# Kernel tuning notes

Measured on AMD Instinct MI355X. Metric: run time of the kernel, lower is better.

## Reference

```python
import jax, jax.numpy as jnp
import numpy as np

B, D, UNITS = 32768, 1024, 1024
NB_FACTOR, SPARSITY = 3, 32
NB = D // SPARSITY  # 32 blocks of 32x32 per block-diagonal factor


def _block_t_matmul(kb, y):
    # kb: [nb, bi, bo] block-diagonal factor values; y: [nb*bi, batch]
    # computes blockdiag(kb)^T @ y without materializing the dense matrix
    nb, bi, bo = kb.shape
    yb = y.reshape(nb, bi, -1)                      # [nb, bi, batch]
    out = jnp.einsum('nio,nib->nob', kb, yb)        # [nb, bo, batch]
    return out.reshape(nb * bo, -1)


def setup_inputs() -> dict:
    key = jax.random.key(0)
    ks = jax.random.split(key, 9)
    return {
        'x': jax.random.normal(ks[0], (B, D), jnp.float32),
        'P0': jax.random.normal(ks[1], (D, D), jnp.float32),
        'P1': jax.random.normal(ks[2], (D, D), jnp.float32),
        'P2': jax.random.normal(ks[3], (D, D), jnp.float32),
        'P3': jax.random.normal(ks[4], (UNITS, UNITS), jnp.float32),
        'K0': jax.random.normal(ks[5], (NB, SPARSITY, SPARSITY), jnp.float32) * 0.05,
        'K1': jax.random.normal(ks[6], (NB, SPARSITY, SPARSITY), jnp.float32) * 0.05,
        'K2': jax.random.normal(ks[7], (NB, SPARSITY, SPARSITY), jnp.float32) * 0.05,
        'bias': jax.random.normal(ks[8], (UNITS,), jnp.float32),
    }


def reference(x, P0, P1, P2, P3, K0, K1, K2, bias):
    # output = (softmax(P3) @ Bd2^T @ softmax(P2) @ Bd1^T @ softmax(P1) @ Bd0^T @ softmax(P0) @ x^T)^T + bias
    y = x.T                                          # [D, B]
    y = jax.nn.softmax(P0, axis=1) @ y
    for kb, perm in ((K0, P1), (K1, P2), (K2, P3)):
        y = _block_t_matmul(kb, y)
        y = jax.nn.softmax(perm, axis=1) @ y
    out = y.T + bias                                 # [B, UNITS]
    return out
```

## Files before the change

kernel.cpp:

```cpp
#include <hip/hip_runtime.h>
#include <hip/hip_bf16.h>

typedef __bf16 bf16x8 __attribute__((ext_vector_type(8)));
typedef float f32x4 __attribute__((ext_vector_type(4)));
typedef unsigned short u16x8 __attribute__((ext_vector_type(8)));

__device__ __forceinline__ unsigned short f2bf(float f) {
  unsigned u = __float_as_uint(f);
  u += 0x7FFF + ((u >> 16) & 1);
  return (unsigned short)(u >> 16);
}
__device__ __forceinline__ float bf2f(unsigned short h) {
  return __uint_as_float((unsigned)h << 16);
}

__device__ __forceinline__ void gload_lds16(const void* g, void* l) {
  __builtin_amdgcn_global_load_lds(
      (const __attribute__((address_space(1))) void*)g,
      (__attribute__((address_space(3))) void*)l, 16, 0, 0);
}

#define LBAR() do { asm volatile("s_waitcnt lgkmcnt(0)" ::: "memory"); \
                    __builtin_amdgcn_s_barrier(); } while (0)

__device__ __forceinline__ void convert_slice(const float* __restrict__ x,
                                              unsigned short* __restrict__ xb,
                                              int base8, int cnt8, int cb, int nb)
{
  int i = cb * 256 + (int)threadIdx.x;
  const int stride = nb * 256;
  for (; i < cnt8; i += stride) {
    const size_t g = (size_t)(base8 + i);
    float4 v0 = ((const float4*)x)[2 * g];
    float4 v1 = ((const float4*)x)[2 * g + 1];
    u16x8 uv;
    uv[0] = f2bf(v0.x); uv[1] = f2bf(v0.y); uv[2] = f2bf(v0.z); uv[3] = f2bf(v0.w);
    uv[4] = f2bf(v1.x); uv[5] = f2bf(v1.y); uv[6] = f2bf(v1.z); uv[7] = f2bf(v1.w);
    ((u16x8*)xb)[g] = uv;
  }
}

__global__ __launch_bounds__(256)
void softmax4_kernel(const float* __restrict__ P0, const float* __restrict__ P1,
                     const float* __restrict__ P2, const float* __restrict__ P3,
                     unsigned short* __restrict__ S,
                     const float* __restrict__ cvx, unsigned short* __restrict__ cvxb,
                     int cvt_cnt)
{
  if (blockIdx.x >= 4096) {
    convert_slice(cvx, cvxb, 0, cvt_cnt, blockIdx.x - 4096, gridDim.x - 4096);
    return;
  }
  const int bid = blockIdx.x;
  const int mat = bid >> 10, row = bid & 1023;
  const float* P = (mat == 0 ? P0 : mat == 1 ? P1 : mat == 2 ? P2 : P3) + (size_t)row * 1024;
  unsigned short* out = S + ((size_t)mat << 20) + (size_t)row * 1024;
  const int t = threadIdx.x, w = t >> 6, l = t & 63;
  float4 v = ((const float4*)P)[t];
  float mx = fmaxf(fmaxf(v.x, v.y), fmaxf(v.z, v.w));
  #pragma unroll
  for (int off = 32; off > 0; off >>= 1) mx = fmaxf(mx, __shfl_xor(mx, off));
  __shared__ float redA[4], redB[4];
  if (l == 0) redA[w] = mx;
  __syncthreads();
  mx = fmaxf(fmaxf(redA[0], redA[1]), fmaxf(redA[2], redA[3]));
  float e0 = __expf(v.x - mx), e1 = __expf(v.y - mx);
  float e2 = __expf(v.z - mx), e3 = __expf(v.w - mx);
  float s = e0 + e1 + e2 + e3;
  #pragma unroll
  for (int off = 32; off > 0; off >>= 1) s += __shfl_xor(s, off);
  if (l == 0) redB[w] = s;
  __syncthreads();
  s = redB[0] + redB[1] + redB[2] + redB[3];
  float inv = 1.0f / s;
  ushort4 o;
  o.x = f2bf(e0 * inv); o.y = f2bf(e1 * inv);
  o.z = f2bf(e2 * inv); o.w = f2bf(e3 * inv);
  ((ushort4*)out)[t] = o;
}

__device__ __forceinline__ void bdT_body(const float* __restrict__ Kb,
                                         const unsigned short* __restrict__ in,
                                         unsigned short* __restrict__ outT, int bid)
{
  const int n = bid >> 2;
  const int c = (bid & 3) * 256 + threadIdx.x;
  __shared__ float Ks[32][33];
  for (int t = threadIdx.x; t < 1024; t += 256)
    Ks[t >> 5][t & 31] = Kb[n * 1024 + t];
  __syncthreads();
  float ri[32];
  #pragma unroll
  for (int i = 0; i < 32; ++i)
    ri[i] = bf2f(in[(size_t)(n * 32 + i) * 1024 + c]);
  unsigned short ov[32];
  #pragma unroll
  for (int o = 0; o < 32; ++o) {
    float acc = 0.f;
    #pragma unroll
    for (int i = 0; i < 32; ++i) acc = fmaf(Ks[i][o], ri[i], acc);
    ov[o] = f2bf(acc);
  }
  u16x8* dst = (u16x8*)(outT + (size_t)c * 1024 + n * 32);
  const u16x8* src = (const u16x8*)ov;
  #pragma unroll
  for (int q = 0; q < 4; ++q) dst[q] = src[q];
}

__global__ __launch_bounds__(256)
void blockdiagT_dual_kernel(const float* Ka, const unsigned short* ina, unsigned short* outa,
                            const float* Kb2, const unsigned short* inb, unsigned short* outb,
                            const float* cvx, unsigned short* cvxb, int cvt_base, int cvt_cnt)
{
  const int bid = blockIdx.x;
  if (bid >= 256) {
    convert_slice(cvx, cvxb, cvt_base, cvt_cnt, bid - 256, gridDim.x - 256);
    return;
  }
  const bool sec = bid >= 128;
  bdT_body(sec ? Kb2 : Ka, sec ? inb : ina, sec ? outb : outa, sec ? bid - 128 : bid);
}

__global__ __launch_bounds__(256)
void bdiag_right_kernel(const float* __restrict__ Kb, const unsigned short* __restrict__ Yt,
                        unsigned short* __restrict__ Zt,
                        const float* cvx, unsigned short* cvxb, int cvt_base, int cvt_cnt)
{
  const int bid = blockIdx.x;
  if (bid >= 256) {
    convert_slice(cvx, cvxb, cvt_base, cvt_cnt, bid - 256, gridDim.x - 256);
    return;
  }
  const int n = bid & 31, rowg = bid >> 5;
  __shared__ float Ks[32][32];
  for (int t = threadIdx.x; t < 1024; t += 256)
    Ks[t >> 5][t & 31] = Kb[n * 1024 + t];
  __syncthreads();
  const int row = rowg * 128 + ((int)threadIdx.x >> 1);
  const int ih = ((int)threadIdx.x & 1) * 16;
  const unsigned short* yrow = Yt + (size_t)row * 1024 + n * 32;
  float y[32];
  #pragma unroll
  for (int q = 0; q < 4; ++q) {
    u16x8 v = ((const u16x8*)yrow)[q];
    #pragma unroll
    for (int e = 0; e < 8; ++e) y[q * 8 + e] = bf2f(v[e]);
  }
  float acc[16] = {};
  #pragma unroll
  for (int o = 0; o < 32; ++o)
    #pragma unroll
    for (int ii = 0; ii < 16; ++ii)
      acc[ii] = fmaf(y[o], Ks[o][ih + ii], acc[ii]);
  u16x8 ov[2];
  #pragma unroll
  for (int ii = 0; ii < 16; ++ii) ov[ii >> 3][ii & 7] = f2bf(acc[ii]);
  u16x8* dst = (u16x8*)(Zt + (size_t)row * 1024 + n * 32 + ih);
  dst[0] = ov[0]; dst[1] = ov[1];
}

template<int TILE, bool A_FP32, bool OUT_BIAS>
__device__ __forceinline__ void gemm_body(const void* __restrict__ Av,
                                          const unsigned short* __restrict__ B,
                                          void* __restrict__ Cv, const float* __restrict__ bias,
                                          int N, int K, int nprim, int bid)
{
  constexpr int FR  = TILE / 32;
  constexpr int SIT = TILE / 32;
  __shared__ unsigned short Asm[TILE * 64];
  __shared__ unsigned short Bsm[TILE * 64];
  const int tid = threadIdx.x;
  const int w = tid >> 6, l = tid & 63;
  const int cpx = nprim >> 3;
  const int swz = (bid & 7) * cpx + (bid >> 3);
  const int ntn = N / TILE;
  const int n0 = (swz % ntn) * TILE;
  const int m0 = (swz / ntn) * TILE;
  const int wr = (w >> 1) * (TILE / 2), wc = (w & 1) * (TILE / 2);
  const int lr = l & 15, kg = (l >> 4) << 3;

  f32x4 acc[FR][FR] = {};
  const int KT = K >> 6;
  for (int kt = 0; kt < KT; ++kt) {
    const int k0 = kt << 6;
    if (kt) __syncthreads();
    #pragma unroll
    for (int it = 0; it < SIT; ++it) {
      int li = it * 256 + tid;
      int row = li >> 3, c8 = (li & 7) << 3;
      const unsigned short* g = B + (size_t)(n0 + row) * K + (k0 + c8);
      gload_lds16(g, (char*)Bsm + it * 4096 + w * 1024);
    }
    if (A_FP32) {
      const float* Af = (const float*)Av;
      #pragma unroll
      for (int p = 0; p < SIT; ++p) {
        int row = (tid >> 3) + p * 32;
        int c8 = (tid & 7) << 3;
        const float* g = Af + (size_t)(m0 + row) * K + (k0 + c8);
        float4 v0 = ((const float4*)g)[0];
        float4 v1 = ((const float4*)g)[1];
        u16x8 uv;
        uv[0] = f2bf(v0.x); uv[1] = f2bf(v0.y); uv[2] = f2bf(v0.z); uv[3] = f2bf(v0.w);
        uv[4] = f2bf(v1.x); uv[5] = f2bf(v1.y); uv[6] = f2bf(v1.z); uv[7] = f2bf(v1.w);
        *(u16x8*)&Asm[row * 64 + c8] = uv;
      }
    } else {
      const unsigned short* Ab = (const unsigned short*)Av;
      #pragma unroll
      for (int it = 0; it < SIT; ++it) {
        int li = it * 256 + tid;
        int row = li >> 3, c8 = (li & 7) << 3;
        const unsigned short* g = Ab + (size_t)(m0 + row) * K + (k0 + c8);
        gload_lds16(g, (char*)Asm + it * 4096 + w * 1024);
      }
    }
    __syncthreads();
    #pragma unroll
    for (int ks = 0; ks < 2; ++ks) {
      const int kb = ks * 32 + kg;
      bf16x8 af[FR], bfr[FR];
      #pragma unroll
      for (int i = 0; i < FR; ++i)
        af[i] = *(const bf16x8*)&Asm[(wr + i * 16 + lr) * 64 + kb];
      #pragma unroll
      for (int j = 0; j < FR; ++j)
        bfr[j] = *(const bf16x8*)&Bsm[(wc + j * 16 + lr) * 64 + kb];
      #pragma unroll
      for (int i = 0; i < FR; ++i)
        #pragma unroll
        for (int j = 0; j < FR; ++j)
          acc[i][j] = __builtin_amdgcn_mfma_f32_16x16x32_bf16(af[i], bfr[j], acc[i][j], 0, 0, 0);
    }
  }
  const int cr = (l >> 4) << 2;
  const int cc = l & 15;
  if (OUT_BIAS) {
    float* C = (float*)Cv;
    #pragma unroll
    for (int j = 0; j < FR; ++j) {
      int col = n0 + wc + j * 16 + cc;
      float bv = bias[col];
      #pragma unroll
      for (int i = 0; i < FR; ++i) {
        int rbase = m0 + wr + i * 16 + cr;
        #pragma unroll
        for (int r = 0; r < 4; ++r)
          C[(size_t)(rbase + r) * N + col] = acc[i][j][r] + bv;
      }
    }
  } else {
    unsigned short* C = (unsigned short*)Cv;
    #pragma unroll
    for (int j = 0; j < FR; ++j) {
      int col = n0 + wc + j * 16 + cc;
      #pragma unroll
      for (int i = 0; i < FR; ++i) {
        int rbase = m0 + wr + i * 16 + cr;
        #pragma unroll
        for (int r = 0; r < 4; ++r)
          C[(size_t)(rbase + r) * N + col] = f2bf(acc[i][j][r]);
      }
    }
  }
}

template<int TILE, bool A_FP32, bool OUT_BIAS>
__global__ __launch_bounds__(256)
void gemm_bt_kernel(const void* __restrict__ Av, const unsigned short* __restrict__ B,
                    void* __restrict__ Cv, const float* __restrict__ bias,
                    int N, int K, int nprim,
                    const float* cvx, unsigned short* cvxb, int cvt_base, int cvt_cnt)
{
  if ((int)blockIdx.x >= nprim) {
    convert_slice(cvx, cvxb, cvt_base, cvt_cnt, blockIdx.x - nprim, gridDim.x - nprim);
    return;
  }
  gemm_body<TILE, A_FP32, OUT_BIAS>(Av, B, Cv, bias, N, K, nprim, blockIdx.x);
}

__global__ __launch_bounds__(256)
void gemm_dual_kernel(const unsigned short* A0, const unsigned short* B0, unsigned short* C0,
                      const unsigned short* A1, const unsigned short* B1, unsigned short* C1,
                      const float* cvx, unsigned short* cvxb, int cvt_base, int cvt_cnt)
{
  const int bid = blockIdx.x;
  if (bid >= 512) {
    convert_slice(cvx, cvxb, cvt_base, cvt_cnt, bid - 512, gridDim.x - 512);
    return;
  }
  const bool sec = bid >= 256;
  gemm_body<64, false, false>(sec ? A1 : A0, sec ? B1 : B0, sec ? (void*)C1 : (void*)C0,
                              nullptr, 1024, 1024, 256, sec ? bid - 256 : bid);
}

template<int QI, int QJ>
__device__ __forceinline__ void phase_compute(const char* Ab, const char* Bb,
    int wm, int wn, int lr, int klo, int sw, f32x4 (&accq)[4][2])
{
  const char* Ah = Ab + QI * 16384;
  const char* Bh = Bb + QJ * 16384;
  #pragma unroll
  for (int ks = 0; ks < 2; ++ks) {
    const int cb = (ks * 64 + klo) ^ sw;
    bf16x8 av[4], bv[2];
    #pragma unroll
    for (int i = 0; i < 4; ++i) {
      const int ra = wm * 64 + i * 16 + lr;
      av[i] = *(const bf16x8*)(Ah + ra * 128 + cb);
    }
    #pragma unroll
    for (int j = 0; j < 2; ++j) {
      const int rb = wn * 32 + j * 16 + lr;
      bv[j] = *(const bf16x8*)(Bh + rb * 128 + cb);
    }
    __builtin_amdgcn_s_setprio(1);
    #pragma unroll
    for (int i = 0; i < 4; ++i)
      #pragma unroll
      for (int j = 0; j < 2; ++j)
        accq[i][j] = __builtin_amdgcn_mfma_f32_16x16x32_bf16(av[i], bv[j], accq[i][j], 0, 0, 0);
    __builtin_amdgcn_s_setprio(0);
  }
}

__global__ __launch_bounds__(512, 2)
void gemm256_kernel(const unsigned short* __restrict__ A,
                    const unsigned short* __restrict__ B,
                    float* __restrict__ C, const float* __restrict__ bias,
                    int N, int K)
{
  extern __shared__ __align__(16) char lds[];
  const int tid = threadIdx.x;
  const int w = tid >> 6, l = tid & 63;
  const int wm = w >> 2, wn = w & 3;
  const int lr = l & 15;
  const int klo = (l >> 4) << 4;
  const int sw  = (lr & 7) << 4;

  const int nwg = gridDim.x;
  const int bid = blockIdx.x;
  const int cpx = nwg >> 3;
  const int swz = (bid & 7) * cpx + (bid >> 3);
  const int ntn = N >> 8;
  const int n0 = (swz % ntn) << 8;
  const int m0 = (swz / ntn) << 8;

  unsigned int aoff[2][2], boff[2][2];
  #pragma unroll
  for (int q = 0; q < 2; ++q)
    #pragma unroll
    for (int it = 0; it < 2; ++it) {
      int L = it * 8192 + tid * 16;
      int r = L >> 7;
      int cs = (L & 127) ^ ((r & 7) << 4);
      aoff[q][it] = (unsigned)(m0 + q * 128 + r) * K + (cs >> 1);
      boff[q][it] = (unsigned)(n0 + q * 128 + r) * K + (cs >> 1);
    }
  char* ldsA = lds;
  char* ldsB = lds + 65536;
  const int wdst = w * 1024;

#define STG_A(bufo, q, k0) do { \
    gload_lds16(A + aoff[q][0] + (k0), ldsA + (bufo) + (q) * 16384 + wdst); \
    gload_lds16(A + aoff[q][1] + (k0), ldsA + (bufo) + (q) * 16384 + 8192 + wdst); } while (0)
#define STG_B(bufo, q, k0) do { \
    gload_lds16(B + boff[q][0] + (k0), ldsB + (bufo) + (q) * 16384 + wdst); \
    gload_lds16(B + boff[q][1] + (k0), ldsB + (bufo) + (q) * 16384 + 8192 + wdst); } while (0)

  f32x4 acc[2][2][4][2] = {};

  STG_A(0, 0, 0); STG_B(0, 0, 0); STG_B(0, 1, 0); STG_A(0, 1, 0);

  const int NT = K >> 6;
  int curo = 0;
  for (int t = 0; t < NT - 1; ++t) {
    const int nxto = curo ^ 32768;
    const int k1 = (t + 1) << 6;
    STG_A(nxto, 0, k1);
    asm volatile("s_waitcnt vmcnt(6)" ::: "memory");
    LBAR();
    phase_compute<0, 0>(ldsA + curo, ldsB + curo, wm, wn, lr, klo, sw, acc[0][0]);
    STG_B(nxto, 0, k1);
    asm volatile("s_waitcnt vmcnt(6)" ::: "memory");
    LBAR();
    phase_compute<0, 1>(ldsA + curo, ldsB + curo, wm, wn, lr, klo, sw, acc[0][1]);
    STG_B(nxto, 1, k1);
    asm volatile("s_waitcnt vmcnt(6)" ::: "memory");
    LBAR();
    phase_compute<1, 0>(ldsA + curo, ldsB + curo, wm, wn, lr, klo, sw, acc[1][0]);
    STG_A(nxto, 1, k1);
    phase_compute<1, 1>(ldsA + curo, ldsB + curo, wm, wn, lr, klo, sw, acc[1][1]);
    curo = nxto;
  }
  asm volatile("s_waitcnt vmcnt(4)" ::: "memory");
  LBAR();
  phase_compute<0, 0>(ldsA + curo, ldsB + curo, wm, wn, lr, klo, sw, acc[0][0]);
  asm volatile("s_waitcnt vmcnt(2)" ::: "memory");
  LBAR();
  phase_compute<0, 1>(ldsA + curo, ldsB + curo, wm, wn, lr, klo, sw, acc[0][1]);
  asm volatile("s_waitcnt vmcnt(0)" ::: "memory");
  LBAR();
  phase_compute<1, 0>(ldsA + curo, ldsB + curo, wm, wn, lr, klo, sw, acc[1][0]);
  phase_compute<1, 1>(ldsA + curo, ldsB + curo, wm, wn, lr, klo, sw, acc[1][1]);

  const int cr = (l >> 4) << 2;
  const int cc = l & 15;
  #pragma unroll
  for (int qi = 0; qi < 2; ++qi)
    #pragma unroll
    for (int qj = 0; qj < 2; ++qj)
      #pragma unroll
      for (int j = 0; j < 2; ++j) {
        const int col = n0 + qj * 128 + wn * 32 + j * 16 + cc;
        const float bv = bias[col];
        #pragma unroll
        for (int i = 0; i < 4; ++i) {
          const int rbase = m0 + qi * 128 + wm * 64 + i * 16 + cr;
          #pragma unroll
          for (int r = 0; r < 4; ++r)
            C[(size_t)(rbase + r) * N + col] = acc[qi][qj][i][j][r] + bv;
        }
      }
#undef STG_A
#undef STG_B
}

extern "C" void kernel_launch(void* const* d_in, const int* in_sizes, int n_in,
                              void* d_out, int out_size, void* d_ws, size_t ws_size,
                              hipStream_t stream) {
  (void)in_sizes; (void)n_in; (void)out_size;
  const float* x    = (const float*)d_in[0];
  const float* P0   = (const float*)d_in[1];
  const float* P1   = (const float*)d_in[2];
  const float* P2   = (const float*)d_in[3];
  const float* P3   = (const float*)d_in[4];
  const float* K0   = (const float*)d_in[5];
  const float* K1   = (const float*)d_in[6];
  const float* K2   = (const float*)d_in[7];
  const float* bias = (const float*)d_in[8];

  unsigned short* S  = (unsigned short*)d_ws;
  unsigned short* s0 = S;
  unsigned short* s1 = S + (1u << 20);
  unsigned short* s2 = S + (2u << 20);
  unsigned short* s3 = S + (3u << 20);
  unsigned short* t0 = S + (4u << 20);
  unsigned short* t1 = S + (5u << 20);
  unsigned short* Xb = S + (6u << 20);
  const size_t need = ((size_t)6 * (1u << 20) + (size_t)32768 * 1024) * 2;
  const bool have_xb = ws_size >= need;
  unsigned short* xbp = have_xb ? Xb : nullptr;

  const int SL = 524288;
  const int cvt2 = have_xb ? 2 * SL : 0;
  const int cvt1 = have_xb ? SL : 0;
  const int tail_smx = have_xb ? 1024 : 0;
  const int tail_512 = have_xb ? 512 : 0;
  const int tail_256 = have_xb ? 256 : 0;

  softmax4_kernel<<<4096 + tail_smx, 256, 0, stream>>>(P0, P1, P2, P3, S, x, xbp, cvt2);

  blockdiagT_dual_kernel<<<256 + tail_512, 256, 0, stream>>>(K2, s2, t0, K0, s0, t1,
                                                             x, xbp, 2 * SL, cvt2);

  gemm_dual_kernel<<<512 + tail_512, 256, 0, stream>>>(s3, t0, s0, t1, s1, s2,
                                                       x, xbp, 4 * SL, cvt2);

  bdiag_right_kernel<<<256 + tail_256, 256, 0, stream>>>(K1, s2, t1, x, xbp, 6 * SL, cvt1);

  gemm_bt_kernel<64, false, false><<<256 + tail_512, 256, 0, stream>>>((const void*)s0, t1,
      (void*)t0, nullptr, 1024, 1024, 256, x, xbp, 7 * SL, cvt1);

  bool ok256 = false;
  if (have_xb) {
    hipError_t e = hipFuncSetAttribute((const void*)gemm256_kernel,
                                       hipFuncAttributeMaxDynamicSharedMemorySize, 131072);
    ok256 = (e == hipSuccess);
  }
  if (ok256) {
    gemm256_kernel<<<512, 512, 131072, stream>>>(Xb, t0, (float*)d_out, bias, 1024, 1024);
  } else if (have_xb) {
    gemm_bt_kernel<128, false, true><<<2048, 256, 0, stream>>>((const void*)Xb, t0,
        d_out, bias, 1024, 1024, 2048, nullptr, nullptr, 0, 0);
  } else {
    gemm_bt_kernel<128, true, true><<<2048, 256, 0, stream>>>((const void*)x, t0,
        d_out, bias, 1024, 1024, 2048, nullptr, nullptr, 0, 0);
  }
}
```

Measured before the change: 161.2 us.

## Merge gemm256 quadrant phases into two, reusing B fragments across A halves

```diff
diff --git a/kernel.cpp b/kernel.cpp
--- a/kernel.cpp
+++ b/kernel.cpp
@@ -294,32 +294,41 @@
                               nullptr, 1024, 1024, 256, sec ? bid - 256 : bid);
 }
 
-template<int QI, int QJ>
-__device__ __forceinline__ void phase_compute(const char* Ab, const char* Bb,
-    int wm, int wn, int lr, int klo, int sw, f32x4 (&accq)[4][2])
-{
-  const char* Ah = Ab + QI * 16384;
-  const char* Bh = Bb + QJ * 16384;
+template<int QI>
+__device__ __forceinline__ void phase_merged(const char* ldsAc, const char* ldsBc,
+    int wm, int wn, int lr, int klo, int sw,
+    bf16x8 (&bv)[2][2][2], f32x4 (&accq)[2][4][2])
+{
+  const char* Ah = ldsAc + QI * 16384;
+  if (QI == 0) {
+    #pragma unroll
+    for (int qj = 0; qj < 2; ++qj) {
+      const char* Bh = ldsBc + qj * 16384;
+      #pragma unroll
+      for (int ks = 0; ks < 2; ++ks) {
+        const int cb = (ks * 64 + klo) ^ sw;
+        #pragma unroll
+        for (int j = 0; j < 2; ++j)
+          bv[qj][j][ks] = *(const bf16x8*)(Bh + (wn * 32 + j * 16 + lr) * 128 + cb);
+      }
+    }
+  }
   #pragma unroll
   for (int ks = 0; ks < 2; ++ks) {
     const int cb = (ks * 64 + klo) ^ sw;
-    bf16x8 av[4], bv[2];
-    #pragma unroll
-    for (int i = 0; i < 4; ++i) {
-      const int ra = wm * 64 + i * 16 + lr;
-      av[i] = *(const bf16x8*)(Ah + ra * 128 + cb);
-    }
-    #pragma unroll
-    for (int j = 0; j < 2; ++j) {
-      const int rb = wn * 32 + j * 16 + lr;
-      bv[j] = *(const bf16x8*)(Bh + rb * 128 + cb);
-    }
+    bf16x8 av[4];
+    #pragma unroll
+    for (int i = 0; i < 4; ++i)
+      av[i] = *(const bf16x8*)(Ah + (wm * 64 + i * 16 + lr) * 128 + cb);
     __builtin_amdgcn_s_setprio(1);
     #pragma unroll
     for (int i = 0; i < 4; ++i)
       #pragma unroll
-      for (int j = 0; j < 2; ++j)
-        accq[i][j] = __builtin_amdgcn_mfma_f32_16x16x32_bf16(av[i], bv[j], accq[i][j], 0, 0, 0);
+      for (int qj = 0; qj < 2; ++qj)
+        #pragma unroll
+        for (int j = 0; j < 2; ++j)
+          accq[qj][i][j] = __builtin_amdgcn_mfma_f32_16x16x32_bf16(av[i], bv[qj][j][ks],
+                                                                  accq[qj][i][j], 0, 0, 0);
     __builtin_amdgcn_s_setprio(0);
   }
 }
@@ -369,6 +378,7 @@
     gload_lds16(B + boff[q][1] + (k0), ldsB + (bufo) + (q) * 16384 + 8192 + wdst); } while (0)
 
   f32x4 acc[2][2][4][2] = {};
+  bf16x8 bv[2][2][2];
 
   STG_A(0, 0, 0); STG_B(0, 0, 0); STG_B(0, 1, 0); STG_A(0, 1, 0);
 
@@ -377,32 +387,22 @@
   for (int t = 0; t < NT - 1; ++t) {
     const int nxto = curo ^ 32768;
     const int k1 = (t + 1) << 6;
-    STG_A(nxto, 0, k1);
+    STG_A(nxto, 0, k1); STG_B(nxto, 0, k1);
     asm volatile("s_waitcnt vmcnt(6)" ::: "memory");
     LBAR();
-    phase_compute<0, 0>(ldsA + curo, ldsB + curo, wm, wn, lr, klo, sw, acc[0][0]);
-    STG_B(nxto, 0, k1);
-    asm volatile("s_waitcnt vmcnt(6)" ::: "memory");
+    phase_merged<0>(ldsA + curo, ldsB + curo, wm, wn, lr, klo, sw, bv, acc[0]);
+    STG_B(nxto, 1, k1); STG_A(nxto, 1, k1);
+    asm volatile("s_waitcnt vmcnt(8)" ::: "memory");
     LBAR();
-    phase_compute<0, 1>(ldsA + curo, ldsB + curo, wm, wn, lr, klo, sw, acc[0][1]);
-    STG_B(nxto, 1, k1);
-    asm volatile("s_waitcnt vmcnt(6)" ::: "memory");
-    LBAR();
-    phase_compute<1, 0>(ldsA + curo, ldsB + curo, wm, wn, lr, klo, sw, acc[1][0]);
-    STG_A(nxto, 1, k1);
-    phase_compute<1, 1>(ldsA + curo, ldsB + curo, wm, wn, lr, klo, sw, acc[1][1]);
+    phase_merged<1>(ldsA + curo, ldsB + curo, wm, wn, lr, klo, sw, bv, acc[1]);
     curo = nxto;
   }
-  asm volatile("s_waitcnt vmcnt(4)" ::: "memory");
-  LBAR();
-  phase_compute<0, 0>(ldsA + curo, ldsB + curo, wm, wn, lr, klo, sw, acc[0][0]);
   asm volatile("s_waitcnt vmcnt(2)" ::: "memory");
   LBAR();
-  phase_compute<0, 1>(ldsA + curo, ldsB + curo, wm, wn, lr, klo, sw, acc[0][1]);
+  phase_merged<0>(ldsA + curo, ldsB + curo, wm, wn, lr, klo, sw, bv, acc[0]);
   asm volatile("s_waitcnt vmcnt(0)" ::: "memory");
   LBAR();
-  phase_compute<1, 0>(ldsA + curo, ldsB + curo, wm, wn, lr, klo, sw, acc[1][0]);
-  phase_compute<1, 1>(ldsA + curo, ldsB + curo, wm, wn, lr, klo, sw, acc[1][1]);
+  phase_merged<1>(ldsA + curo, ldsB + curo, wm, wn, lr, klo, sw, bv, acc[1]);
 
   const int cr = (l >> 4) << 2;
   const int cc = l & 15;
@@ -413,13 +413,13 @@
       #pragma unroll
       for (int j = 0; j < 2; ++j) {
         const int col = n0 + qj * 128 + wn * 32 + j * 16 + cc;
-        const float bv = bias[col];
+        const float bvv = bias[col];
         #pragma unroll
         for (int i = 0; i < 4; ++i) {
           const int rbase = m0 + qi * 128 + wm * 64 + i * 16 + cr;
           #pragma unroll
           for (int r = 0; r < 4; ++r)
-            C[(size_t)(rbase + r) * N + col] = acc[qi][qj][i][j][r] + bv;
+            C[(size_t)(rbase + r) * N + col] = acc[qi][qj][i][j][r] + bvv;
         }
       }
 #undef STG_A
```

After: 159.4 us. No clear change (-1.1%).
